# Performance work log

Hardware: AMD Instinct MI355X
Metric: run time of the kernel (lower is better)

## Reference

```python
import jax, jax.numpy as jnp
import numpy as np
import math

EPS = 1e-9
NORM = 1.0 / math.sqrt(20.0)  # num_neighbours=20 default


def _mixing(x1, x2, B, W, b):
    # nn.Bilinear (no bias): x_bi[n,k] = sum_ij x1[n,i] B[k,i,j] x2[n,j]
    x_bi = jnp.einsum('ni,kij->nkj', x1, B)
    x_bi = jnp.einsum('nkj,nj->nk', x_bi, x2)
    x = jnp.concatenate([x1, x2, x_bi], axis=-1)
    return x @ W.T + b


def _rowstd(x):
    # torch.std default: unbiased (ddof=1)
    return jnp.std(x, axis=1, ddof=1, keepdims=True)


def setup_inputs() -> dict:
    key = jax.random.key(0)
    N, E = 100000, 2000000
    DN, DE, DA_N, DA_E = 32, 32, 3, 1
    ks = jax.random.split(key, 24)

    def nrm(k, shape, fan_in):
        return jax.random.normal(k, shape, dtype=jnp.float32) / np.sqrt(fan_in)

    inp = {
        'xn': jax.random.normal(ks[0], (N, DN), dtype=jnp.float32),
        'xn_attr': jax.random.normal(ks[1], (N, DA_N), dtype=jnp.float32),
        'xe_attr': jax.random.normal(ks[2], (E, DA_E), dtype=jnp.float32),
        'xe_src': jax.random.randint(ks[3], (E,), 0, N),
        'xe_dst': jax.random.randint(ks[4], (E,), 0, N),
        # fc1: Linear(1, xe_dim); fc2: Linear(1, xn_dim)
        'W_fc1': nrm(ks[5], (DE, 1), 1), 'b_fc1': jnp.zeros((DE,), jnp.float32),
        'W_fc2': nrm(ks[6], (DN, 1), 1), 'b_fc2': jnp.zeros((DN,), jnp.float32),
        # mix_xn: Mixing(DN, DA_N, DN)
        'B_mix_xn': nrm(ks[7], (DN, DN, DA_N), DN * DA_N),
        'W_mix_xn': nrm(ks[8], (DN, 2 * DN + DA_N), 2 * DN + DA_N),
        'b_mix_xn': jnp.zeros((DN,), jnp.float32),
        # nodes_to_edges.mix: Mixing(DN, DN, DN)
        'B_n2e': nrm(ks[9], (DN, DN, DN), DN * DN),
        'W_n2e': nrm(ks[10], (DN, 3 * DN), 3 * DN),
        'b_n2e': jnp.zeros((DN,), jnp.float32),
        # mix_xe: Mixing(DE, DA_E, DE)
        'B_mix_xe': nrm(ks[11], (DE, DE, DA_E), DE * DA_E),
        'W_mix_xe': nrm(ks[12], (DE, 2 * DE + DA_E), 2 * DE + DA_E),
        'b_mix_xe': jnp.zeros((DE,), jnp.float32),
        # edges_to_nodes.mix: Mixing(DE, DE, DE)
        'B_e2n': nrm(ks[13], (DE, DE, DE), DE * DE),
        'W_e2n': nrm(ks[14], (DE, 3 * DE), 3 * DE),
        'b_e2n': jnp.zeros((DE,), jnp.float32),
    }
    return inp


def reference(xn, xn_attr, xe_attr, xe_src, xe_dst,
              W_fc1, b_fc1, W_fc2, b_fc2,
              B_mix_xn, W_mix_xn, b_mix_xn,
              B_n2e, W_n2e, b_n2e,
              B_mix_xe, W_mix_xe, b_mix_xe,
              B_e2n, W_e2n, b_e2n):
    n_nodes = xn.shape[0]
    # node mixing + per-row std norm
    xn = _mixing(xn, xn_attr, B_mix_xn, W_mix_xn, b_mix_xn)
    xn = xn / (_rowstd(xn) + EPS)
    # fc1 weight: [E, xe_dim]
    w1 = jax.nn.silu(xe_attr @ W_fc1.T + b_fc1)
    # NodesToEdges: gather -> grad/ave -> mixing
    xg, xd = xn[xe_src], xn[xe_dst]
    xe = _mixing(w1 * (xg - xd), w1 * (xg + xd) * 0.5, B_n2e, W_n2e, b_n2e)
    xe = _mixing(xe, xe_attr, B_mix_xe, W_mix_xe, b_mix_xe)
    xe = xe / (_rowstd(xe) + EPS)
    # fc2 weight: [E, xn_dim]
    w2 = jax.nn.silu(xe_attr @ W_fc2.T + b_fc2)
    # EdgesToNodes: scatter-add over dst/src, diff/sum, mixing
    wxe = w2 * xe
    xn1 = jax.ops.segment_sum(wxe, xe_dst, num_segments=n_nodes) * NORM
    xn2 = jax.ops.segment_sum(wxe, xe_src, num_segments=n_nodes) * NORM
    xn = _mixing(xn1 - xn2, xn1 + xn2, B_e2n, W_e2n, b_e2n)
    xn = jax.nn.silu(xn)
    xn = xn / (_rowstd(xn) + EPS)
    return xn
```

## Files before the change

kernel.cpp:

```cpp
#include <hip/hip_runtime.h>
#include <hip/hip_bf16.h>

#define N_NODES 100000
#define N_EDGES 2000000
#define EPS 1e-9f
#define NORMC 0.22360679774997896f

#define BKSZ   256
#define NBK1   391
#define NBK    782
#define NSB    256
#define CE     7813
#define NITEMS 4000000

typedef short s8 __attribute__((ext_vector_type(8)));
typedef float f4 __attribute__((ext_vector_type(4)));

__device__ __forceinline__ float silu_f(float x) {
    return x / (1.0f + __expf(-x));
}

__device__ __forceinline__ ushort f2bfu(float f) {
    union { __hip_bfloat16 b; ushort u; } cv;
    cv.b = __float2bfloat16(f);
    return cv.u;
}

__device__ __forceinline__ uint pkbf(float lo, float hi) {
    float2 t; t.x = lo; t.y = hi;
    union { __hip_bfloat162 b; uint u; } cv;
    cv.b = __float22bfloat162_rn(t);
    return cv.u;
}


__device__ float mext(const float* __restrict__ W, const float* __restrict__ B,
                      const float* __restrict__ bias, int n, int i, int j) {
    if (i < 32 && j < 32) {
        float r = 0.f;
        #pragma unroll
        for (int m = 0; m < 32; ++m) r += W[n*96 + 64 + m] * B[m*1024 + i*32 + j];
        return r;
    }
    if (i < 32) return W[n*96 + i];
    if (j < 32) return W[n*96 + 32 + j];
    return bias[n];
}

__global__ void prep_kernel(const float* __restrict__ W_n2e, const float* __restrict__ B_n2e,
                            const float* __restrict__ b_n2e,
                            const float* __restrict__ W_e2n, const float* __restrict__ B_e2n,
                            const float* __restrict__ b_e2n,
                            const float* __restrict__ W_mix_xn, const float* __restrict__ B_mix_xn,
                            const float* __restrict__ b_mix_xn,
                            const float* __restrict__ W_mix_xe, const float* __restrict__ B_mix_xe,
                            const float* __restrict__ b_mix_xe,
                            ushort* __restrict__ MF, ushort* __restrict__ MG,
                            float* __restrict__ BpN, float* __restrict__ WxE,
                            float* __restrict__ CtE) {
    int t = blockIdx.x * blockDim.x + threadIdx.x;
    if (t < 69632) {
        int u = (t < 34816) ? t : t - 34816;
        int tt = u & 7, lane = (u >> 3) & 63, rest = u >> 9;
        int nt = rest & 1, kk = rest >> 1;
        int n = nt*16 + (lane & 15);
        int kl = ((lane >> 4) & 3) * 8 + tt;
        int i, j;
        if (kk < 33) { i = kk; j = kl; } else { i = kl; j = 32; }
        if (t < 34816) MF[u] = f2bfu(mext(W_n2e, B_n2e, b_n2e, n, i, j));
        else           MG[u] = f2bfu(mext(W_e2n, B_e2n, b_e2n, n, i, j));
    } else if (t < 73856) {
        int u = t - 69632;
        int k = u & 31, ij = u >> 5;
        int i = ij >> 2, j = ij & 3;
        float r;
        if (i < 32 && j < 3) {
            r = 0.f;
            #pragma unroll
            for (int m = 0; m < 32; ++m) r += W_mix_xn[k*67 + 35 + m] * B_mix_xn[m*96 + i*3 + j];
        } else if (i < 32 && j == 3) {
            r = W_mix_xn[k*67 + i];
        } else if (i == 32 && j < 3) {
            r = W_mix_xn[k*67 + 32 + j];
        } else {
            r = b_mix_xn[k];
        }
        BpN[ij*32 + k] = r;
    } else if (t < 74912) {
        int u = t - 73856;
        int k = u & 31, i = u >> 5;
        WxE[i*32 + k] = (i < 32) ? W_mix_xe[k*65 + i] : b_mix_xe[k];
    } else if (t < 75968) {
        int u = t - 74912;
        int k = u & 31, i = u >> 5;
        float r;
        if (i < 32) {
            r = 0.f;
            #pragma unroll
            for (int m = 0; m < 32; ++m) r += W_mix_xe[k*65 + 33 + m] * B_mix_xe[m*32 + i];
        } else {
            r = W_mix_xe[k*65 + 32];
        }
        CtE[i*32 + k] = r;
    }
}

__global__ void zero_kernel(float4* __restrict__ p, int n4) {
    int i = blockIdx.x * blockDim.x + threadIdx.x;
    int stride = gridDim.x * blockDim.x;
    float4 z = {0.f, 0.f, 0.f, 0.f};
    for (; i < n4; i += stride) p[i] = z;
}

__global__ __launch_bounds__(256) void node_kernel(
    const float* __restrict__ xn, const float* __restrict__ xn_attr,
    const float* __restrict__ BpN, float* __restrict__ xn_norm) {
    int n = blockIdx.x * 256 + threadIdx.x;
    if (n >= N_NODES) return;
    float x[33];
    const float4* xr = (const float4*)(xn + (size_t)n * 32);
    #pragma unroll
    for (int q = 0; q < 8; ++q) {
        float4 v = xr[q];
        x[q*4+0] = v.x; x[q*4+1] = v.y; x[q*4+2] = v.z; x[q*4+3] = v.w;
    }
    x[32] = 1.f;
    float at[4];
    at[0] = xn_attr[n*3]; at[1] = xn_attr[n*3+1]; at[2] = xn_attr[n*3+2]; at[3] = 1.f;

    float acc[32];
    #pragma unroll
    for (int k = 0; k < 32; ++k) acc[k] = 0.f;
    #pragma unroll
    for (int i = 0; i < 33; ++i) {
        #pragma unroll
        for (int j = 0; j < 4; ++j) {
            float s = x[i] * at[j];
            const float* bp = BpN + (i*4 + j) * 32;
            #pragma unroll
            for (int k = 0; k < 32; ++k) acc[k] = fmaf(bp[k], s, acc[k]);
        }
    }
    float mean = 0.f;
    #pragma unroll
    for (int k = 0; k < 32; ++k) mean += acc[k];
    mean *= (1.0f / 32.0f);
    float var = 0.f;
    #pragma unroll
    for (int k = 0; k < 32; ++k) { float d = acc[k] - mean; var += d * d; }
    var *= (1.0f / 31.0f);
    float inv = 1.0f / (sqrtf(var) + EPS);
    float4* out = (float4*)(xn_norm + (size_t)n * 32);
    #pragma unroll
    for (int q = 0; q < 8; ++q) {
        float4 v;
        v.x = acc[q*4+0]*inv; v.y = acc[q*4+1]*inv; v.z = acc[q*4+2]*inv; v.w = acc[q*4+3]*inv;
        out[q] = v;
    }
}


__global__ __launch_bounds__(256) void count_kernel(
    const int* __restrict__ xe_src, const int* __restrict__ xe_dst,
    int* __restrict__ cntg) {
    __shared__ int cnt[NBK];
    int tid = threadIdx.x, b = blockIdx.x;
    for (int k = tid; k < NBK; k += 256) cnt[k] = 0;
    __syncthreads();
    int e0 = b * CE;
    for (int i = tid; i < CE; i += 256) {
        int e = e0 + i;
        if (e < N_EDGES) {
            atomicAdd(&cnt[xe_dst[e] >> 8], 1);
            atomicAdd(&cnt[NBK1 + (xe_src[e] >> 8)], 1);
        }
    }
    __syncthreads();
    for (int k = tid; k < NBK; k += 256) cntg[k * NSB + b] = cnt[k];
}

#define SCAN_TOT (NBK * NSB)

__global__ __launch_bounds__(1024) void scan_kernel(
    const int* __restrict__ cntg, int* __restrict__ scang) {
    __shared__ int part[1024];
    int t = threadIdx.x;
    const int CHUNK = 196;
    int base = t * CHUNK;
    int s = 0;
    for (int i = 0; i < CHUNK; ++i) {
        int idx = base + i;
        if (idx < SCAN_TOT) s += cntg[idx];
    }
    part[t] = s;
    __syncthreads();
    for (int off = 1; off < 1024; off <<= 1) {
        int v = part[t];
        int add = (t >= off) ? part[t - off] : 0;
        __syncthreads();
        part[t] = v + add;
        __syncthreads();
    }
    int run = (t == 0) ? 0 : part[t - 1];
    for (int i = 0; i < CHUNK; ++i) {
        int idx = base + i;
        if (idx < SCAN_TOT) {
            int c = cntg[idx];
            scang[idx] = run;
            run += c;
        }
    }
}

__global__ __launch_bounds__(256) void scatter_kernel(
    const int* __restrict__ xe_src, const int* __restrict__ xe_dst,
    const int* __restrict__ scang, int* __restrict__ bucketed) {
    __shared__ int cur[NBK];
    int tid = threadIdx.x, b = blockIdx.x;
    for (int k = tid; k < NBK; k += 256) cur[k] = scang[k * NSB + b];
    __syncthreads();
    int e0 = b * CE;
    for (int i = tid; i < CE; i += 256) {
        int e = e0 + i;
        if (e < N_EDGES) {
            int d = xe_dst[e];
            int p = atomicAdd(&cur[d >> 8], 1);
            bucketed[p] = e | ((d & 255) << 21);
            int s_ = xe_src[e];
            p = atomicAdd(&cur[NBK1 + (s_ >> 8)], 1);
            bucketed[p] = e | ((s_ & 255) << 21);
        }
    }
}

__global__ __launch_bounds__(256) void gather_kernel(
    const ushort* __restrict__ wxe, const int* __restrict__ bucketed,
    const int* __restrict__ scang, float* __restrict__ sd0) {
    __shared__ float accs[BKSZ * 33];
    int tid = threadIdx.x, bk = blockIdx.x;
    for (int i = tid; i < BKSZ * 33; i += 256) accs[i] = 0.f;
    __syncthreads();
    int start = scang[bk * NSB];
    int end = (bk == NBK - 1) ? NITEMS : scang[(bk + 1) * NSB];
    int q = tid >> 2, g = tid & 3;
    uint4 z4; z4.x = 0u; z4.y = 0u; z4.z = 0u; z4.w = 0u;

    int i0 = start + q;
    int p0 = (i0 < end) ? bucketed[i0] : 0;
    int p1 = (i0 + 64 < end) ? bucketed[i0 + 64] : 0;
    uint4 r0 = (i0 < end)
             ? *(const uint4*)(wxe + (size_t)(p0 & 0x1FFFFF) * 32 + g * 8) : z4;

    for (int i = i0; i < end; i += 64) {
        int pn = (i + 128 < end) ? bucketed[i + 128] : 0;
        uint4 r1 = (i + 64 < end)
                 ? *(const uint4*)(wxe + (size_t)(p1 & 0x1FFFFF) * 32 + g * 8) : z4;
        int ln = (p0 >> 21) & 255;
        float* ap = &accs[ln * 33 + g * 8];
        uint uu[4] = {r0.x, r0.y, r0.z, r0.w};
        #pragma unroll
        for (int c = 0; c < 4; ++c) {
            uint u = uu[c];
            atomicAdd(&ap[c*2],     __uint_as_float((u & 0xFFFFu) << 16));
            atomicAdd(&ap[c*2 + 1], __uint_as_float(u & 0xFFFF0000u));
        }
        p0 = p1; p1 = pn; r0 = r1;
    }
    __syncthreads();
    int side = (bk < NBK1) ? 0 : 1;
    int nb = side ? bk - NBK1 : bk;
    float* out = sd0 + (size_t)side * 3211264 + (size_t)nb * BKSZ * 32;
    for (int i = tid; i < BKSZ * 32; i += 256) {
        int node = i >> 5, k = i & 31;
        out[i] = accs[node * 33 + k];
    }
}


__device__ __forceinline__ void gemm33(const ushort* __restrict__ sM,
                                       float* __restrict__ a_f,
                                       const ushort* __restrict__ ab,
                                       const float* __restrict__ biasv, int tid) {
    int lane = tid & 63, wv = tid >> 6;
    int m = lane & 15, h = lane >> 4;
    int base = wv * 64;
    float bfv[4][8];
    s8 araw[4];
    #pragma unroll
    for (int g = 0; g < 4; ++g) {
        const ushort* rp = &ab[(size_t)(base + g*16 + m) * 72];
        union { s8 v; ushort s[8]; } braw;
        braw.v = *(const s8*)&rp[h*8];
        #pragma unroll
        for (int t = 0; t < 8; ++t) {
            union { uint u; float f; } cv; cv.u = ((uint)braw.s[t]) << 16;
            bfv[g][t] = cv.f;
        }
        araw[g] = *(const s8*)&rp[32 + h*8];
    }
    f4 c[4][2];
    #pragma unroll
    for (int g = 0; g < 4; ++g) {
        c[g][0] = (f4){0.f, 0.f, 0.f, 0.f};
        c[g][1] = (f4){0.f, 0.f, 0.f, 0.f};
    }
    const s8* M8 = (const s8*)sM;
    #pragma unroll
    for (int kk = 0; kk < 33; ++kk) {
        s8 mf0 = M8[(kk*2 + 0)*64 + lane];
        s8 mf1 = M8[(kk*2 + 1)*64 + lane];
        #pragma unroll
        for (int g = 0; g < 4; ++g) {
            float as = a_f[(size_t)(base + g*16 + m) * 33 + kk];
            union { s8 v; uint u[4]; } af;
            #pragma unroll
            for (int t = 0; t < 4; ++t) af.u[t] = pkbf(as * bfv[g][2*t], as * bfv[g][2*t+1]);
            c[g][0] = __builtin_amdgcn_mfma_f32_16x16x32_bf16(af.v, mf0, c[g][0], 0, 0, 0);
            c[g][1] = __builtin_amdgcn_mfma_f32_16x16x32_bf16(af.v, mf1, c[g][1], 0, 0, 0);
        }
    }
    {
        s8 mf0 = M8[66*64 + lane];
        s8 mf1 = M8[67*64 + lane];
        #pragma unroll
        for (int g = 0; g < 4; ++g) {
            c[g][0] = __builtin_amdgcn_mfma_f32_16x16x32_bf16(araw[g], mf0, c[g][0], 0, 0, 0);
            c[g][1] = __builtin_amdgcn_mfma_f32_16x16x32_bf16(araw[g], mf1, c[g][1], 0, 0, 0);
        }
    }
    float b0 = biasv[m], b1 = biasv[16 + m];
    #pragma unroll
    for (int g = 0; g < 4; ++g) {
        int rowb = base + g*16 + h*4;
        #pragma unroll
        for (int r = 0; r < 4; ++r) {
            a_f[(size_t)(rowb + r) * 33 + m]      = c[g][0][r] + b0;
            a_f[(size_t)(rowb + r) * 33 + 16 + m] = c[g][1][r] + b1;
        }
    }
}

#define TILES_E 7813

template<bool STORE>
__global__ __launch_bounds__(256, 1) void edge_kernel(
    const float* __restrict__ xn_norm, const float* __restrict__ xe_attr,
    const int* __restrict__ xe_src, const int* __restrict__ xe_dst,
    const float* __restrict__ W_fc1, const float* __restrict__ b_fc1,
    const float* __restrict__ W_fc2, const float* __restrict__ b_fc2,
    const ushort* __restrict__ MF, const float* __restrict__ biasE,
    const float* __restrict__ WxE, const float* __restrict__ CtE,
    float* __restrict__ acc1, float* __restrict__ acc2,
    ushort* __restrict__ wxe) {
    __shared__ __align__(16) ushort sM[34816];
    __shared__ __align__(16) float  a_f[256 * 33];
    __shared__ __align__(16) ushort ab[256 * 72];
    int tid = threadIdx.x;
    {
        const float4* s4p = (const float4*)MF;
        float4* d4p = (float4*)sM;
        #pragma unroll
        for (int i = 0; i < 17; ++i) d4p[tid + i*256] = s4p[tid + i*256];
    }
    uint* ab32 = (uint*)ab;

    int t = blockIdx.x;
    float attrP = 0.f; int srcP = 0, dstP = 0; bool okP = false;
    float4 gP[8], dP[8];
    {
        int e = t*256 + tid;
        okP = e < N_EDGES;
        int ec = okP ? e : 0;
        attrP = xe_attr[ec]; srcP = xe_src[ec]; dstP = xe_dst[ec];
        const float4* gp = (const float4*)(xn_norm + (size_t)srcP * 32);
        const float4* dp = (const float4*)(xn_norm + (size_t)dstP * 32);
        #pragma unroll
        for (int q = 0; q < 8; ++q) { gP[q] = gp[q]; dP[q] = dp[q]; }
    }

    for (; t < TILES_E; t += 256) {
        float attr = attrP; int csrc = srcP, cdst = dstP; bool okC = okP;
        float vs = okC ? 1.f : 0.f;
        #pragma unroll
        for (int q = 0; q < 8; ++q) {
            float4 g = gP[q], d = dP[q];
            float gg[4] = {g.x, g.y, g.z, g.w};
            float dd[4] = {d.x, d.y, d.z, d.w};
            #pragma unroll
            for (int p = 0; p < 2; ++p) {
                int k = q*4 + p*2;
                float w0 = silu_f(attr * W_fc1[k]   + b_fc1[k])   * vs;
                float w1 = silu_f(attr * W_fc1[k+1] + b_fc1[k+1]) * vs;
                float av0 = w0 * (gg[2*p]   - dd[2*p]);
                float av1 = w1 * (gg[2*p+1] - dd[2*p+1]);
                float bv0 = w0 * (gg[2*p]   + dd[2*p])   * 0.5f;
                float bv1 = w1 * (gg[2*p+1] + dd[2*p+1]) * 0.5f;
                a_f[tid*33 + k]   = av0;
                a_f[tid*33 + k+1] = av1;
                ab32[tid*36 + (k>>1)]      = pkbf(bv0, bv1);
                ab32[tid*36 + 16 + (k>>1)] = pkbf(av0, av1);
            }
        }
        a_f[tid*33 + 32] = 1.f;

        int tn = t + 256;
        if (tn < TILES_E) {
            int e = tn*256 + tid;
            okP = e < N_EDGES;
            int ec = okP ? e : 0;
            attrP = xe_attr[ec]; srcP = xe_src[ec]; dstP = xe_dst[ec];
            const float4* gp = (const float4*)(xn_norm + (size_t)srcP * 32);
            const float4* dp = (const float4*)(xn_norm + (size_t)dstP * 32);
            #pragma unroll
            for (int q = 0; q < 8; ++q) { gP[q] = gp[q]; dP[q] = dp[q]; }
        }
        __syncthreads();

        gemm33(sM, a_f, ab, biasE, tid);
        __syncthreads();

        float2 y2[16];
        #pragma unroll
        for (int k2 = 0; k2 < 16; ++k2) y2[k2] = make_float2(0.f, 0.f);
        for (int i = 0; i < 33; ++i) {
            float xi = a_f[tid*33 + i];
            const float2* wx2 = (const float2*)(WxE + i * 32);
            const float2* ct2 = (const float2*)(CtE + i * 32);
            #pragma unroll
            for (int k2 = 0; k2 < 16; ++k2) {
                float2 w = wx2[k2], ctv = ct2[k2];
                float lx = fmaf(attr, ctv.x, w.x);
                float ly = fmaf(attr, ctv.y, w.y);
                y2[k2].x = fmaf(lx, xi, y2[k2].x);
                y2[k2].y = fmaf(ly, xi, y2[k2].y);
            }
        }
        float mean = 0.f;
        #pragma unroll
        for (int k2 = 0; k2 < 16; ++k2) mean += y2[k2].x + y2[k2].y;
        mean *= (1.0f / 32.0f);
        float var = 0.f;
        #pragma unroll
        for (int k2 = 0; k2 < 16; ++k2) {
            float dx = y2[k2].x - mean, dy = y2[k2].y - mean;
            var += dx*dx + dy*dy;
        }
        var *= (1.0f / 31.0f);
        float inv = 1.0f / (sqrtf(var) + EPS);

        if (okC) {
            if (STORE) {
                uint pkv[16];
                #pragma unroll
                for (int k2 = 0; k2 < 16; ++k2) {
                    float w20 = silu_f(attr * W_fc2[2*k2]   + b_fc2[2*k2]);
                    float w21 = silu_f(attr * W_fc2[2*k2+1] + b_fc2[2*k2+1]);
                    pkv[k2] = pkbf(w20 * y2[k2].x * inv, w21 * y2[k2].y * inv);
                }
                uint4* wp = (uint4*)(wxe + (size_t)(t*256 + tid) * 32);
                #pragma unroll
                for (int q = 0; q < 4; ++q) {
                    uint4 v; v.x = pkv[q*4]; v.y = pkv[q*4+1]; v.z = pkv[q*4+2]; v.w = pkv[q*4+3];
                    wp[q] = v;
                }
            } else {
                float* p1 = acc1 + (size_t)cdst * 32;
                float* p2 = acc2 + (size_t)csrc * 32;
                #pragma unroll
                for (int k = 0; k < 32; ++k) {
                    float yk = (k & 1) ? y2[k>>1].y : y2[k>>1].x;
                    float w2 = silu_f(attr * W_fc2[k] + b_fc2[k]);
                    float v = w2 * yk * inv;
                    unsafeAtomicAdd(p1 + k, v);
                    unsafeAtomicAdd(p2 + k, v);
                }
            }
        }
    }
}

#define TILES_F 391

__global__ __launch_bounds__(256, 1) void final_kernel(
    const float* __restrict__ acc1, const float* __restrict__ acc2,
    const ushort* __restrict__ MG, const float* __restrict__ biasG,
    float* __restrict__ out) {
    __shared__ __align__(16) ushort sM[34816];
    __shared__ __align__(16) float  a_f[256 * 33];
    __shared__ __align__(16) ushort ab[256 * 72];
    int tid = threadIdx.x;
    {
        const float4* s4p = (const float4*)MG;
        float4* d4p = (float4*)sM;
        #pragma unroll
        for (int i = 0; i < 17; ++i) d4p[tid + i*256] = s4p[tid + i*256];
    }
    uint* ab32 = (uint*)ab;

    for (int t = blockIdx.x; t < TILES_F; t += 256) {
        int n = t*256 + tid;
        bool ok = n < N_NODES;
        int nn = ok ? n : 0;
        float vs = ok ? 1.f : 0.f;
        const float4* p1 = (const float4*)(acc1 + (size_t)nn * 32);
        const float4* p2 = (const float4*)(acc2 + (size_t)nn * 32);
        #pragma unroll
        for (int q = 0; q < 8; ++q) {
            float4 u1 = p1[q], u2 = p2[q];
            float a1[4] = {u1.x, u1.y, u1.z, u1.w};
            float a2[4] = {u2.x, u2.y, u2.z, u2.w};
            #pragma unroll
            for (int p = 0; p < 2; ++p) {
                int k = q*4 + p*2;
                float dv0 = (a1[2*p]   - a2[2*p])   * NORMC * vs;
                float dv1 = (a1[2*p+1] - a2[2*p+1]) * NORMC * vs;
                float sv0 = (a1[2*p]   + a2[2*p])   * NORMC * vs;
                float sv1 = (a1[2*p+1] + a2[2*p+1]) * NORMC * vs;
                a_f[tid*33 + k]   = dv0;
                a_f[tid*33 + k+1] = dv1;
                ab32[tid*36 + (k>>1)]      = pkbf(sv0, sv1);
                ab32[tid*36 + 16 + (k>>1)] = pkbf(dv0, dv1);
            }
        }
        a_f[tid*33 + 32] = 1.f;
        __syncthreads();

        gemm33(sM, a_f, ab, biasG, tid);
        __syncthreads();

        if (ok) {
            float z[32];
            float mean = 0.f;
            #pragma unroll
            for (int k = 0; k < 32; ++k) { z[k] = silu_f(a_f[tid*33 + k]); mean += z[k]; }
            mean *= (1.0f / 32.0f);
            float var = 0.f;
            #pragma unroll
            for (int k = 0; k < 32; ++k) { float d = z[k] - mean; var += d * d; }
            var *= (1.0f / 31.0f);
            float inv = 1.0f / (sqrtf(var) + EPS);
            float4* op = (float4*)(out + (size_t)n * 32);
            #pragma unroll
            for (int q = 0; q < 8; ++q) {
                float4 v;
                v.x = z[q*4+0]*inv; v.y = z[q*4+1]*inv; v.z = z[q*4+2]*inv; v.w = z[q*4+3]*inv;
                op[q] = v;
            }
        }
    }
}

extern "C" void kernel_launch(void* const* d_in, const int* in_sizes, int n_in,
                              void* d_out, int out_size, void* d_ws, size_t ws_size,
                              hipStream_t stream) {
    const float* xn       = (const float*)d_in[0];
    const float* xn_attr  = (const float*)d_in[1];
    const float* xe_attr  = (const float*)d_in[2];
    const int*   xe_src   = (const int*)d_in[3];
    const int*   xe_dst   = (const int*)d_in[4];
    const float* W_fc1    = (const float*)d_in[5];
    const float* b_fc1    = (const float*)d_in[6];
    const float* W_fc2    = (const float*)d_in[7];
    const float* b_fc2    = (const float*)d_in[8];
    const float* B_mix_xn = (const float*)d_in[9];
    const float* W_mix_xn = (const float*)d_in[10];
    const float* b_mix_xn = (const float*)d_in[11];
    const float* B_n2e    = (const float*)d_in[12];
    const float* W_n2e    = (const float*)d_in[13];
    const float* b_n2e    = (const float*)d_in[14];
    const float* B_mix_xe = (const float*)d_in[15];
    const float* W_mix_xe = (const float*)d_in[16];
    const float* b_mix_xe = (const float*)d_in[17];
    const float* B_e2n    = (const float*)d_in[18];
    const float* W_e2n    = (const float*)d_in[19];
    const float* b_e2n    = (const float*)d_in[20];

    float* ws = (float*)d_ws;
    const size_t MAIN_BYTES = 46065088ULL * 4ULL;
    bool big = ws_size >= MAIN_BYTES;

    if (big) {
        float*  xn_norm = ws;
        float*  sd0     = ws + 3200000;
        float*  sd1     = ws + 6411264;
        ushort* MF      = (ushort*)(ws + 9622528);
        ushort* MG      = MF + 34816;
        float*  BpN     = ws + 9657344;
        float*  WxE     = ws + 9661568;
        float*  CtE     = ws + 9662624;
        ushort* wxe     = (ushort*)(ws + 9663680);
        int*    bucketed= (int*)(ws + 41663680);
        int*    cntg    = (int*)(ws + 45663680);
        int*    scang   = (int*)(ws + 45864384);

        prep_kernel<<<297, 256, 0, stream>>>(W_n2e, B_n2e, b_n2e, W_e2n, B_e2n, b_e2n,
                                             W_mix_xn, B_mix_xn, b_mix_xn,
                                             W_mix_xe, B_mix_xe, b_mix_xe,
                                             MF, MG, BpN, WxE, CtE);
        node_kernel<<<391, 256, 0, stream>>>(xn, xn_attr, BpN, xn_norm);
        count_kernel<<<NSB, 256, 0, stream>>>(xe_src, xe_dst, cntg);
        scan_kernel<<<1, 1024, 0, stream>>>(cntg, scang);
        scatter_kernel<<<NSB, 256, 0, stream>>>(xe_src, xe_dst, scang, bucketed);
        edge_kernel<true><<<256, 256, 0, stream>>>(xn_norm, xe_attr, xe_src, xe_dst,
                                                   W_fc1, b_fc1, W_fc2, b_fc2,
                                                   MF, b_n2e, WxE, CtE,
                                                   nullptr, nullptr, wxe);
        gather_kernel<<<NBK, 256, 0, stream>>>(wxe, bucketed, scang, sd0);
        final_kernel<<<391, 256, 0, stream>>>(sd0, sd1, MG, b_e2n, (float*)d_out);
    } else {
        float*  xn_norm = ws;
        float*  acc1    = ws + 3200000;
        float*  acc2    = ws + 6400000;
        ushort* MF      = (ushort*)(ws + 9600000);
        ushort* MG      = MF + 34816;
        float*  BpN     = ws + 9600000 + 34816;
        float*  WxE     = BpN + 4224;
        float*  CtE     = WxE + 1056;

        prep_kernel<<<297, 256, 0, stream>>>(W_n2e, B_n2e, b_n2e, W_e2n, B_e2n, b_e2n,
                                             W_mix_xn, B_mix_xn, b_mix_xn,
                                             W_mix_xe, B_mix_xe, b_mix_xe,
                                             MF, MG, BpN, WxE, CtE);
        zero_kernel<<<2048, 256, 0, stream>>>((float4*)acc1, 1600000);
        node_kernel<<<391, 256, 0, stream>>>(xn, xn_attr, BpN, xn_norm);
        edge_kernel<false><<<256, 256, 0, stream>>>(xn_norm, xe_attr, xe_src, xe_dst,
                                                    W_fc1, b_fc1, W_fc2, b_fc2,
                                                    MF, b_n2e, WxE, CtE,
                                                    acc1, acc2, nullptr);
        final_kernel<<<391, 256, 0, stream>>>(acc1, acc2, MG, b_e2n, (float*)d_out);
    }
}
```

Baseline: 2.013 ms.

## Process edges in dst-sorted order with in-block dst accumulation and src-ordered output

The edge kernel now walks edges sorted by destination bucket, accumulating the dst-side scatter in shared memory and flushing per bucket with atomics. Its wxe output is written directly in src-bucket order, so the src-side gather streams contiguously instead of reading through an index. The bilinear GEMM also stops storing a bf16 copy of the grad operand and converts it from fp32 on the fly. The cost is more random reads of edge attributes and node rows via the sort permutation, plus per-tile block-wide min/sync loops for bucket changes.

```diff
diff --git a/kernel.cpp b/kernel.cpp
--- a/kernel.cpp
+++ b/kernel.cpp
@@ -9,9 +9,11 @@
 #define BKSZ   256
 #define NBK1   391
 #define NBK    782
-#define NSB    256
-#define CE     7813
-#define NITEMS 4000000
+#define NSB    320
+#define CE     6250
+#define SCAN_TOT (NBK * NSB)
+#define TILES_E 7813
+#define TPB_E   31
 
 typedef short s8 __attribute__((ext_vector_type(8)));
 typedef float f4 __attribute__((ext_vector_type(4)));
@@ -179,13 +181,10 @@
     for (int k = tid; k < NBK; k += 256) cntg[k * NSB + b] = cnt[k];
 }
 
-#define SCAN_TOT (NBK * NSB)
-
-__global__ __launch_bounds__(1024) void scan_kernel(
-    const int* __restrict__ cntg, int* __restrict__ scang) {
+__global__ __launch_bounds__(1024) void scan_kernel(int* __restrict__ cntg) {
     __shared__ int part[1024];
     int t = threadIdx.x;
-    const int CHUNK = 196;
+    const int CHUNK = 245;
     int base = t * CHUNK;
     int s = 0;
     for (int i = 0; i < CHUNK; ++i) {
@@ -206,7 +205,7 @@
         int idx = base + i;
         if (idx < SCAN_TOT) {
             int c = cntg[idx];
-            scang[idx] = run;
+            cntg[idx] = run;
             run += c;
         }
     }
@@ -214,7 +213,8 @@
 
 __global__ __launch_bounds__(256) void scatter_kernel(
     const int* __restrict__ xe_src, const int* __restrict__ xe_dst,
-    const int* __restrict__ scang, int* __restrict__ bucketed) {
+    const int* __restrict__ scang, int* __restrict__ esort,
+    int* __restrict__ possrc, unsigned char* __restrict__ srcln) {
     __shared__ int cur[NBK];
     int tid = threadIdx.x, b = blockIdx.x;
     for (int k = tid; k < NBK; k += 256) cur[k] = scang[k * NSB + b];
@@ -225,38 +225,35 @@
         if (e < N_EDGES) {
             int d = xe_dst[e];
             int p = atomicAdd(&cur[d >> 8], 1);
-            bucketed[p] = e | ((d & 255) << 21);
+            esort[p] = e;
             int s_ = xe_src[e];
-            p = atomicAdd(&cur[NBK1 + (s_ >> 8)], 1);
-            bucketed[p] = e | ((s_ & 255) << 21);
-        }
-    }
-}
-
-__global__ __launch_bounds__(256) void gather_kernel(
-    const ushort* __restrict__ wxe, const int* __restrict__ bucketed,
-    const int* __restrict__ scang, float* __restrict__ sd0) {
+            int p2 = atomicAdd(&cur[NBK1 + (s_ >> 8)], 1) - N_EDGES;
+            possrc[e] = p2;
+            srcln[p2] = (unsigned char)(s_ & 255);
+        }
+    }
+}
+
+__global__ __launch_bounds__(256) void gather_stream(
+    const ushort* __restrict__ wxe2, const unsigned char* __restrict__ srcln,
+    const int* __restrict__ scang, float* __restrict__ sd1) {
     __shared__ float accs[BKSZ * 33];
     int tid = threadIdx.x, bk = blockIdx.x;
     for (int i = tid; i < BKSZ * 33; i += 256) accs[i] = 0.f;
     __syncthreads();
-    int start = scang[bk * NSB];
-    int end = (bk == NBK - 1) ? NITEMS : scang[(bk + 1) * NSB];
+    int start = scang[(NBK1 + bk) * NSB] - N_EDGES;
+    int end = (bk == NBK1 - 1) ? N_EDGES : scang[(NBK1 + bk + 1) * NSB] - N_EDGES;
     int q = tid >> 2, g = tid & 3;
     uint4 z4; z4.x = 0u; z4.y = 0u; z4.z = 0u; z4.w = 0u;
 
     int i0 = start + q;
-    int p0 = (i0 < end) ? bucketed[i0] : 0;
-    int p1 = (i0 + 64 < end) ? bucketed[i0 + 64] : 0;
-    uint4 r0 = (i0 < end)
-             ? *(const uint4*)(wxe + (size_t)(p0 & 0x1FFFFF) * 32 + g * 8) : z4;
-
+    int ln0 = (i0 < end) ? (int)srcln[i0] : 0;
+    uint4 r0 = (i0 < end) ? *(const uint4*)(wxe2 + (size_t)i0 * 32 + g * 8) : z4;
     for (int i = i0; i < end; i += 64) {
-        int pn = (i + 128 < end) ? bucketed[i + 128] : 0;
-        uint4 r1 = (i + 64 < end)
-                 ? *(const uint4*)(wxe + (size_t)(p1 & 0x1FFFFF) * 32 + g * 8) : z4;
-        int ln = (p0 >> 21) & 255;
-        float* ap = &accs[ln * 33 + g * 8];
+        int in = i + 64;
+        int ln1 = (in < end) ? (int)srcln[in] : 0;
+        uint4 r1 = (in < end) ? *(const uint4*)(wxe2 + (size_t)in * 32 + g * 8) : z4;
+        float* ap = &accs[ln0 * 33 + g * 8];
         uint uu[4] = {r0.x, r0.y, r0.z, r0.w};
         #pragma unroll
         for (int c = 0; c < 4; ++c) {
@@ -264,18 +261,15 @@
             atomicAdd(&ap[c*2],     __uint_as_float((u & 0xFFFFu) << 16));
             atomicAdd(&ap[c*2 + 1], __uint_as_float(u & 0xFFFF0000u));
         }
-        p0 = p1; p1 = pn; r0 = r1;
+        ln0 = ln1; r0 = r1;
     }
     __syncthreads();
-    int side = (bk < NBK1) ? 0 : 1;
-    int nb = side ? bk - NBK1 : bk;
-    float* out = sd0 + (size_t)side * 3211264 + (size_t)nb * BKSZ * 32;
-    for (int i = tid; i < BKSZ * 32; i += 256) {
-        int node = i >> 5, k = i & 31;
-        out[i] = accs[node * 33 + k];
-    }
-}
-
+    float* out = sd1 + (size_t)bk * BKSZ * 32;
+    for (int i2 = tid; i2 < BKSZ * 32; i2 += 256) {
+        int node = i2 >> 5, k = i2 & 31;
+        out[i2] = accs[node * 33 + k];
+    }
+}
 
 __device__ __forceinline__ void gemm33(const ushort* __restrict__ sM,
                                        float* __restrict__ a_f,
@@ -285,18 +279,15 @@
     int m = lane & 15, h = lane >> 4;
     int base = wv * 64;
     float bfv[4][8];
-    s8 araw[4];
     #pragma unroll
     for (int g = 0; g < 4; ++g) {
-        const ushort* rp = &ab[(size_t)(base + g*16 + m) * 72];
         union { s8 v; ushort s[8]; } braw;
-        braw.v = *(const s8*)&rp[h*8];
+        braw.v = *(const s8*)&ab[(size_t)(base + g*16 + m) * 40 + h*8];
         #pragma unroll
         for (int t = 0; t < 8; ++t) {
             union { uint u; float f; } cv; cv.u = ((uint)braw.s[t]) << 16;
             bfv[g][t] = cv.f;
         }
-        araw[g] = *(const s8*)&rp[32 + h*8];
     }
     f4 c[4][2];
     #pragma unroll
@@ -324,8 +315,12 @@
         s8 mf1 = M8[67*64 + lane];
         #pragma unroll
         for (int g = 0; g < 4; ++g) {
-            c[g][0] = __builtin_amdgcn_mfma_f32_16x16x32_bf16(araw[g], mf0, c[g][0], 0, 0, 0);
-            c[g][1] = __builtin_amdgcn_mfma_f32_16x16x32_bf16(araw[g], mf1, c[g][1], 0, 0, 0);
+            const float* arow = &a_f[(size_t)(base + g*16 + m) * 33 + h*8];
+            union { s8 v; uint u[4]; } af;
+            #pragma unroll
+            for (int t = 0; t < 4; ++t) af.u[t] = pkbf(arow[2*t], arow[2*t+1]);
+            c[g][0] = __builtin_amdgcn_mfma_f32_16x16x32_bf16(af.v, mf0, c[g][0], 0, 0, 0);
+            c[g][1] = __builtin_amdgcn_mfma_f32_16x16x32_bf16(af.v, mf1, c[g][1], 0, 0, 0);
         }
     }
     float b0 = biasv[m], b1 = biasv[16 + m];
@@ -340,21 +335,201 @@
     }
 }
 
-#define TILES_E 7813
-
-template<bool STORE>
-__global__ __launch_bounds__(256, 1) void edge_kernel(
+__device__ __forceinline__ float mixe_std(const float* __restrict__ a_f, int tid,
+                                          float attr,
+                                          const float* __restrict__ WxE,
+                                          const float* __restrict__ CtE,
+                                          float2* __restrict__ y2) {
+    #pragma unroll
+    for (int k2 = 0; k2 < 16; ++k2) y2[k2] = make_float2(0.f, 0.f);
+    for (int i = 0; i < 33; ++i) {
+        float xi = a_f[tid*33 + i];
+        const float2* wx2 = (const float2*)(WxE + i * 32);
+        const float2* ct2 = (const float2*)(CtE + i * 32);
+        #pragma unroll
+        for (int k2 = 0; k2 < 16; ++k2) {
+            float2 w = wx2[k2], ctv = ct2[k2];
+            float lx = fmaf(attr, ctv.x, w.x);
+            float ly = fmaf(attr, ctv.y, w.y);
+            y2[k2].x = fmaf(lx, xi, y2[k2].x);
+            y2[k2].y = fmaf(ly, xi, y2[k2].y);
+        }
+    }
+    float mean = 0.f;
+    #pragma unroll
+    for (int k2 = 0; k2 < 16; ++k2) mean += y2[k2].x + y2[k2].y;
+    mean *= (1.0f / 32.0f);
+    float var = 0.f;
+    #pragma unroll
+    for (int k2 = 0; k2 < 16; ++k2) {
+        float dx = y2[k2].x - mean, dy = y2[k2].y - mean;
+        var += dx*dx + dy*dy;
+    }
+    var *= (1.0f / 31.0f);
+    return 1.0f / (sqrtf(var) + EPS);
+}
+
+__global__ __launch_bounds__(256, 1) void edge_sorted(
     const float* __restrict__ xn_norm, const float* __restrict__ xe_attr,
     const int* __restrict__ xe_src, const int* __restrict__ xe_dst,
     const float* __restrict__ W_fc1, const float* __restrict__ b_fc1,
     const float* __restrict__ W_fc2, const float* __restrict__ b_fc2,
     const ushort* __restrict__ MF, const float* __restrict__ biasE,
     const float* __restrict__ WxE, const float* __restrict__ CtE,
-    float* __restrict__ acc1, float* __restrict__ acc2,
-    ushort* __restrict__ wxe) {
+    const int* __restrict__ esort, const int* __restrict__ possrc,
+    ushort* __restrict__ wxe2, float* __restrict__ sd0) {
     __shared__ __align__(16) ushort sM[34816];
     __shared__ __align__(16) float  a_f[256 * 33];
-    __shared__ __align__(16) ushort ab[256 * 72];
+    __shared__ __align__(16) ushort ab[256 * 40];
+    __shared__ float accs[BKSZ * 33];
+    __shared__ int s_min, s_cb;
+    int tid = threadIdx.x;
+    int t0 = blockIdx.x * TPB_E;
+    int t1 = (t0 + TPB_E < TILES_E) ? t0 + TPB_E : TILES_E;
+    if (t0 >= TILES_E) return;
+    {
+        const float4* s4p = (const float4*)MF;
+        float4* d4p = (float4*)sM;
+        #pragma unroll
+        for (int i = 0; i < 17; ++i) d4p[tid + i*256] = s4p[tid + i*256];
+    }
+    for (int i = tid; i < BKSZ * 33; i += 256) accs[i] = 0.f;
+    uint* ab32 = (uint*)ab;
+
+    float attrC = 0.f; int srcC = 0, dstC = 0, posC = 0; bool okC = false;
+    float4 gC[8], dC[8];
+    {
+        int gi = t0*256 + tid;
+        okC = gi < N_EDGES;
+        int e = esort[okC ? gi : N_EDGES - 1];
+        attrC = xe_attr[e]; srcC = xe_src[e]; dstC = xe_dst[e]; posC = possrc[e];
+        const float4* gp = (const float4*)(xn_norm + (size_t)srcC * 32);
+        const float4* dp = (const float4*)(xn_norm + (size_t)dstC * 32);
+        #pragma unroll
+        for (int q = 0; q < 8; ++q) { gC[q] = gp[q]; dC[q] = dp[q]; }
+    }
+    if (tid == 0) s_cb = xe_dst[esort[t0 * 256]] >> 8;
+    __syncthreads();
+    int cb = s_cb;
+
+    float attrN; int srcN, dstN, posN; bool okN = false;
+    float4 gN[8], dN[8];
+
+    for (int t = t0; t < t1; ++t) {
+        float attr = attrC; int cdst = dstC, cpos = posC; bool ok = okC;
+        float vs = ok ? 1.f : 0.f;
+        #pragma unroll
+        for (int q = 0; q < 8; ++q) {
+            float4 g = gC[q], d = dC[q];
+            float gg[4] = {g.x, g.y, g.z, g.w};
+            float dd[4] = {d.x, d.y, d.z, d.w};
+            #pragma unroll
+            for (int p = 0; p < 2; ++p) {
+                int k = q*4 + p*2;
+                float w0 = silu_f(attr * W_fc1[k]   + b_fc1[k])   * vs;
+                float w1 = silu_f(attr * W_fc1[k+1] + b_fc1[k+1]) * vs;
+                float av0 = w0 * (gg[2*p]   - dd[2*p]);
+                float av1 = w1 * (gg[2*p+1] - dd[2*p+1]);
+                float bv0 = w0 * (gg[2*p]   + dd[2*p])   * 0.5f;
+                float bv1 = w1 * (gg[2*p+1] + dd[2*p+1]) * 0.5f;
+                a_f[tid*33 + k]   = av0;
+                a_f[tid*33 + k+1] = av1;
+                ab32[tid*20 + (k>>1)] = pkbf(bv0, bv1);
+            }
+        }
+        a_f[tid*33 + 32] = 1.f;
+
+        if (t + 1 < t1) {
+            int gi = (t+1)*256 + tid;
+            okN = gi < N_EDGES;
+            int e = esort[okN ? gi : N_EDGES - 1];
+            attrN = xe_attr[e]; srcN = xe_src[e]; dstN = xe_dst[e]; posN = possrc[e];
+            const float4* gp = (const float4*)(xn_norm + (size_t)srcN * 32);
+            const float4* dp = (const float4*)(xn_norm + (size_t)dstN * 32);
+            #pragma unroll
+            for (int q = 0; q < 8; ++q) { gN[q] = gp[q]; dN[q] = dp[q]; }
+        }
+        __syncthreads();
+
+        gemm33(sM, a_f, ab, biasE, tid);
+        __syncthreads();
+
+        float2 y2[16];
+        float inv = mixe_std(a_f, tid, attr, WxE, CtE, y2);
+
+        float val[32];
+        uint pkv[16];
+        #pragma unroll
+        for (int k2 = 0; k2 < 16; ++k2) {
+            float w20 = silu_f(attr * W_fc2[2*k2]   + b_fc2[2*k2]);
+            float w21 = silu_f(attr * W_fc2[2*k2+1] + b_fc2[2*k2+1]);
+            float v0 = w20 * y2[k2].x * inv;
+            float v1 = w21 * y2[k2].y * inv;
+            val[2*k2] = v0; val[2*k2+1] = v1;
+            pkv[k2] = pkbf(v0, v1);
+        }
+        if (ok) {
+            uint4* wp = (uint4*)(wxe2 + (size_t)cpos * 32);
+            #pragma unroll
+            for (int q = 0; q < 4; ++q) {
+                uint4 v; v.x = pkv[q*4]; v.y = pkv[q*4+1]; v.z = pkv[q*4+2]; v.w = pkv[q*4+3];
+                wp[q] = v;
+            }
+        }
+        int myb = ok ? (cdst >> 8) : 0x7FFFFFFF;
+        int ln = cdst & 255;
+        bool pend = ok;
+        for (;;) {
+            if (tid == 0) s_min = 0x7FFFFFFF;
+            __syncthreads();
+            if (pend) atomicMin(&s_min, myb);
+            __syncthreads();
+            int mb = s_min;
+            if (mb == 0x7FFFFFFF) break;
+            if (mb != cb) {
+                for (int i = tid; i < BKSZ * 32; i += 256) {
+                    int nn = i >> 5, k = i & 31;
+                    float v = accs[nn*33 + k];
+                    int node = cb * 256 + nn;
+                    if (v != 0.f && node < N_NODES)
+                        unsafeAtomicAdd(&sd0[(size_t)node*32 + k], v);
+                    accs[nn*33 + k] = 0.f;
+                }
+                cb = mb;
+                __syncthreads();
+            }
+            if (pend && myb == cb) {
+                float* ap = &accs[ln * 33];
+                #pragma unroll
+                for (int k = 0; k < 32; ++k) atomicAdd(&ap[k], val[k]);
+                pend = false;
+            }
+        }
+        attrC = attrN; srcC = srcN; dstC = dstN; posC = posN; okC = okN;
+        #pragma unroll
+        for (int q = 0; q < 8; ++q) { gC[q] = gN[q]; dC[q] = dN[q]; }
+    }
+    __syncthreads();
+    for (int i = tid; i < BKSZ * 32; i += 256) {
+        int nn = i >> 5, k = i & 31;
+        float v = accs[nn*33 + k];
+        int node = cb * 256 + nn;
+        if (v != 0.f && node < N_NODES)
+            unsafeAtomicAdd(&sd0[(size_t)node*32 + k], v);
+    }
+}
+
+__global__ __launch_bounds__(256, 1) void edge_atomic(
+    const float* __restrict__ xn_norm, const float* __restrict__ xe_attr,
+    const int* __restrict__ xe_src, const int* __restrict__ xe_dst,
+    const float* __restrict__ W_fc1, const float* __restrict__ b_fc1,
+    const float* __restrict__ W_fc2, const float* __restrict__ b_fc2,
+    const ushort* __restrict__ MF, const float* __restrict__ biasE,
+    const float* __restrict__ WxE, const float* __restrict__ CtE,
+    float* __restrict__ acc1, float* __restrict__ acc2) {
+    __shared__ __align__(16) ushort sM[34816];
+    __shared__ __align__(16) float  a_f[256 * 33];
+    __shared__ __align__(16) ushort ab[256 * 40];
     int tid = threadIdx.x;
     {
         const float4* s4p = (const float4*)MF;
@@ -397,8 +572,7 @@
                 float bv1 = w1 * (gg[2*p+1] + dd[2*p+1]) * 0.5f;
                 a_f[tid*33 + k]   = av0;
                 a_f[tid*33 + k+1] = av1;
-                ab32[tid*36 + (k>>1)]      = pkbf(bv0, bv1);
-                ab32[tid*36 + 16 + (k>>1)] = pkbf(av0, av1);
+                ab32[tid*20 + (k>>1)] = pkbf(bv0, bv1);
             }
         }
         a_f[tid*33 + 32] = 1.f;
@@ -420,60 +594,18 @@
         __syncthreads();
 
         float2 y2[16];
-        #pragma unroll
-        for (int k2 = 0; k2 < 16; ++k2) y2[k2] = make_float2(0.f, 0.f);
-        for (int i = 0; i < 33; ++i) {
-            float xi = a_f[tid*33 + i];
-            const float2* wx2 = (const float2*)(WxE + i * 32);
-            const float2* ct2 = (const float2*)(CtE + i * 32);
-            #pragma unroll
-            for (int k2 = 0; k2 < 16; ++k2) {
-                float2 w = wx2[k2], ctv = ct2[k2];
-                float lx = fmaf(attr, ctv.x, w.x);
-                float ly = fmaf(attr, ctv.y, w.y);
-                y2[k2].x = fmaf(lx, xi, y2[k2].x);
-                y2[k2].y = fmaf(ly, xi, y2[k2].y);
-            }
-        }
-        float mean = 0.f;
-        #pragma unroll
-        for (int k2 = 0; k2 < 16; ++k2) mean += y2[k2].x + y2[k2].y;
-        mean *= (1.0f / 32.0f);
-        float var = 0.f;
-        #pragma unroll
-        for (int k2 = 0; k2 < 16; ++k2) {
-            float dx = y2[k2].x - mean, dy = y2[k2].y - mean;
-            var += dx*dx + dy*dy;
-        }
-        var *= (1.0f / 31.0f);
-        float inv = 1.0f / (sqrtf(var) + EPS);
+        float inv = mixe_std(a_f, tid, attr, WxE, CtE, y2);
 
         if (okC) {
-            if (STORE) {
-                uint pkv[16];
-                #pragma unroll
-                for (int k2 = 0; k2 < 16; ++k2) {
-                    float w20 = silu_f(attr * W_fc2[2*k2]   + b_fc2[2*k2]);
-                    float w21 = silu_f(attr * W_fc2[2*k2+1] + b_fc2[2*k2+1]);
-                    pkv[k2] = pkbf(w20 * y2[k2].x * inv, w21 * y2[k2].y * inv);
-                }
-                uint4* wp = (uint4*)(wxe + (size_t)(t*256 + tid) * 32);
-                #pragma unroll
-                for (int q = 0; q < 4; ++q) {
-                    uint4 v; v.x = pkv[q*4]; v.y = pkv[q*4+1]; v.z = pkv[q*4+2]; v.w = pkv[q*4+3];
-                    wp[q] = v;
-                }
-            } else {
-                float* p1 = acc1 + (size_t)cdst * 32;
-                float* p2 = acc2 + (size_t)csrc * 32;
-                #pragma unroll
-                for (int k = 0; k < 32; ++k) {
-                    float yk = (k & 1) ? y2[k>>1].y : y2[k>>1].x;
-                    float w2 = silu_f(attr * W_fc2[k] + b_fc2[k]);
-                    float v = w2 * yk * inv;
-                    unsafeAtomicAdd(p1 + k, v);
-                    unsafeAtomicAdd(p2 + k, v);
-                }
+            float* p1 = acc1 + (size_t)cdst * 32;
+            float* p2 = acc2 + (size_t)csrc * 32;
+            #pragma unroll
+            for (int k = 0; k < 32; ++k) {
+                float yk = (k & 1) ? y2[k>>1].y : y2[k>>1].x;
+                float w2 = silu_f(attr * W_fc2[k] + b_fc2[k]);
+                float vv = w2 * yk * inv;
+                unsafeAtomicAdd(p1 + k, vv);
+                unsafeAtomicAdd(p2 + k, vv);
             }
         }
     }
@@ -487,7 +619,7 @@
     float* __restrict__ out) {
     __shared__ __align__(16) ushort sM[34816];
     __shared__ __align__(16) float  a_f[256 * 33];
-    __shared__ __align__(16) ushort ab[256 * 72];
+    __shared__ __align__(16) ushort ab[256 * 40];
     int tid = threadIdx.x;
     {
         const float4* s4p = (const float4*)MG;
@@ -518,8 +650,7 @@
                 float sv1 = (a1[2*p+1] + a2[2*p+1]) * NORMC * vs;
                 a_f[tid*33 + k]   = dv0;
                 a_f[tid*33 + k+1] = dv1;
-                ab32[tid*36 + (k>>1)]      = pkbf(sv0, sv1);
-                ab32[tid*36 + 16 + (k>>1)] = pkbf(dv0, dv1);
+                ab32[tid*20 + (k>>1)] = pkbf(sv0, sv1);
             }
         }
         a_f[tid*33 + 32] = 1.f;
@@ -576,36 +707,38 @@
     const float* b_e2n    = (const float*)d_in[20];
 
     float* ws = (float*)d_ws;
-    const size_t MAIN_BYTES = 46065088ULL * 4ULL;
-    bool big = ws_size >= MAIN_BYTES;
-
-    if (big) {
+    const size_t T1_BYTES = 46394464ULL * 4ULL;
+
+    if (ws_size >= T1_BYTES) {
         float*  xn_norm = ws;
         float*  sd0     = ws + 3200000;
-        float*  sd1     = ws + 6411264;
-        ushort* MF      = (ushort*)(ws + 9622528);
-        ushort* MG      = MF + 34816;
-        float*  BpN     = ws + 9657344;
-        float*  WxE     = ws + 9661568;
-        float*  CtE     = ws + 9662624;
-        ushort* wxe     = (ushort*)(ws + 9663680);
-        int*    bucketed= (int*)(ws + 41663680);
-        int*    cntg    = (int*)(ws + 45663680);
-        int*    scang   = (int*)(ws + 45864384);
+        float*  sd1     = ws + 6400000;
+        ushort* MF      = (ushort*)(ws + 9603072);
+        ushort* MG      = (ushort*)(ws + 9620480);
+        float*  BpN     = ws + 9637888;
+        float*  WxE     = ws + 9642112;
+        float*  CtE     = ws + 9643168;
+        ushort* wxe2    = (ushort*)(ws + 9644224);
+        int*    esort   = (int*)(ws + 41644224);
+        int*    possrc  = (int*)(ws + 43644224);
+        unsigned char* srcln = (unsigned char*)(ws + 45644224);
+        int*    cntg    = (int*)(ws + 46144224);
 
         prep_kernel<<<297, 256, 0, stream>>>(W_n2e, B_n2e, b_n2e, W_e2n, B_e2n, b_e2n,
                                              W_mix_xn, B_mix_xn, b_mix_xn,
                                              W_mix_xe, B_mix_xe, b_mix_xe,
                                              MF, MG, BpN, WxE, CtE);
+        zero_kernel<<<2048, 256, 0, stream>>>((float4*)sd0, 800000);
         node_kernel<<<391, 256, 0, stream>>>(xn, xn_attr, BpN, xn_norm);
         count_kernel<<<NSB, 256, 0, stream>>>(xe_src, xe_dst, cntg);
-        scan_kernel<<<1, 1024, 0, stream>>>(cntg, scang);
-        scatter_kernel<<<NSB, 256, 0, stream>>>(xe_src, xe_dst, scang, bucketed);
-        edge_kernel<true><<<256, 256, 0, stream>>>(xn_norm, xe_attr, xe_src, xe_dst,
-                                                   W_fc1, b_fc1, W_fc2, b_fc2,
-                                                   MF, b_n2e, WxE, CtE,
-                                                   nullptr, nullptr, wxe);
-        gather_kernel<<<NBK, 256, 0, stream>>>(wxe, bucketed, scang, sd0);
+        scan_kernel<<<1, 1024, 0, stream>>>(cntg);
+        scatter_kernel<<<NSB, 256, 0, stream>>>(xe_src, xe_dst, cntg,
+                                                esort, possrc, srcln);
+        edge_sorted<<<256, 256, 0, stream>>>(xn_norm, xe_attr, xe_src, xe_dst,
+                                             W_fc1, b_fc1, W_fc2, b_fc2,
+                                             MF, b_n2e, WxE, CtE,
+                                             esort, possrc, wxe2, sd0);
+        gather_stream<<<NBK1, 256, 0, stream>>>(wxe2, srcln, cntg, sd1);
         final_kernel<<<391, 256, 0, stream>>>(sd0, sd1, MG, b_e2n, (float*)d_out);
     } else {
         float*  xn_norm = ws;
@@ -623,10 +756,9 @@
                                              MF, MG, BpN, WxE, CtE);
         zero_kernel<<<2048, 256, 0, stream>>>((float4*)acc1, 1600000);
         node_kernel<<<391, 256, 0, stream>>>(xn, xn_attr, BpN, xn_norm);
-        edge_kernel<false><<<256, 256, 0, stream>>>(xn_norm, xe_attr, xe_src, xe_dst,
-                                                    W_fc1, b_fc1, W_fc2, b_fc2,
-                                                    MF, b_n2e, WxE, CtE,
-                                                    acc1, acc2, nullptr);
+        edge_atomic<<<256, 256, 0, stream>>>(xn_norm, xe_attr, xe_src, xe_dst,
+                                             W_fc1, b_fc1, W_fc2, b_fc2,
+                                             MF, b_n2e, WxE, CtE, acc1, acc2);
         final_kernel<<<391, 256, 0, stream>>>(acc1, acc2, MG, b_e2n, (float*)d_out);
     }
 }
```

After: 2.211 ms. 9.9% more time.
